# Kernel optimization log

Hardware: AMD Instinct MI355X
Metric: run time of the kernel (lower is better)

The kernel has to match this reference:

```python
import jax, jax.numpy as jnp
import numpy as np

T, A, H = 1024, 64, 2048

def setup_inputs() -> dict:
    key = jax.random.key(0)
    ks = jax.random.split(key, 12)
    s = 0.02
    return {
        "actions": jax.random.normal(ks[0], (T, A), jnp.float32),
        "state": jnp.zeros((1, H), jnp.float32),
        "W_ih": jax.random.normal(ks[1], (3 * H, A), jnp.float32) * s,
        "W_hh": jax.random.normal(ks[2], (3 * H, H), jnp.float32) * s,
        "b_ih": jax.random.normal(ks[3], (3 * H,), jnp.float32) * s,
        "b_hh": jax.random.normal(ks[4], (3 * H,), jnp.float32) * s,
        "fc1_w": jax.random.normal(ks[5], (H, H), jnp.float32) * s,
        "fc1_b": jax.random.normal(ks[6], (H,), jnp.float32) * s,
        "fc2_w": jax.random.normal(ks[7], (H, H), jnp.float32) * s,
        "fc2_b": jax.random.normal(ks[8], (H,), jnp.float32) * s,
        "mean_w": jax.random.normal(ks[9], (H, H), jnp.float32) * s,
        "mean_b": jnp.zeros((H,), jnp.float32),
        "std_w": jax.random.normal(ks[10], (H, H), jnp.float32) * s,
        "std_b": jnp.zeros((H,), jnp.float32),
    }

def reference(actions, state, W_ih, W_hh, b_ih, b_hh, fc1_w, fc1_b, fc2_w, fc2_b, mean_w, mean_b, std_w, std_b):
    def step(h, x):
        # torch GRUCell gate order: r, z, n
        gi = x[None] @ W_ih.T + b_ih          # [1, 3H]
        gh = h @ W_hh.T + b_hh                # [1, 3H]
        i_r, i_z, i_n = jnp.split(gi, 3, axis=-1)
        h_r, h_z, h_n = jnp.split(gh, 3, axis=-1)
        r = jax.nn.sigmoid(i_r + h_r)
        z = jax.nn.sigmoid(i_z + h_z)
        n = jnp.tanh(i_n + r * h_n)
        h_new = (1.0 - z) * n + z * h         # [1, H]
        s = jax.nn.elu(h_new)
        s = jax.nn.elu(s @ fc1_w.T + fc1_b)
        s = jax.nn.elu(s @ fc2_w.T + fc2_b)   # carried state for next step
        m = (s @ mean_w.T + mean_b)[0]        # [H]
        sd = jax.nn.softplus(s @ std_w.T + std_b)[0]
        return s, (m, sd)

    _, (means, stds) = jax.lax.scan(step, state, actions)
    return means, stds  # Normal(means, stds) parameters, each [T, H]
```

## Files before the change

kernel.cpp:

```cpp
#include <hip/hip_runtime.h>
#include <hip/hip_bf16.h>
#include <math.h>

#define T_STEPS 1024
#define HDIM    2048
#define ADIM    64
#define NBLK    256
#define NTHR    512
#define WPB     (NTHR / 64)

__device__ __forceinline__ float elu_f(float x)      { return x > 0.f ? x : expm1f(x); }
__device__ __forceinline__ float sigmoid_f(float x)  { return 1.f / (1.f + expf(-x)); }
__device__ __forceinline__ float softplus_f(float x) { return x > 0.f ? x + log1pf(expf(-x)) : log1pf(expf(x)); }

__device__ __forceinline__ unsigned long long cload64(const unsigned long long* p) {
    return __hip_atomic_load(p, __ATOMIC_RELAXED, __HIP_MEMORY_SCOPE_AGENT);
}
__device__ __forceinline__ void cstore64(unsigned long long* p, unsigned long long v) {
    __hip_atomic_store(p, v, __ATOMIC_RELAXED, __HIP_MEMORY_SCOPE_AGENT);
}
__device__ __forceinline__ unsigned long long pack_tag(unsigned tag, float v) {
    return ((unsigned long long)tag << 32) | (unsigned long long)__float_as_uint(v);
}

__device__ __forceinline__ void consume_vec(const unsigned long long* __restrict__ tg,
                                            unsigned tag, float* __restrict__ lsv) {
    const int i = threadIdx.x;
    unsigned pend = 0xFu;
    while (pend) {
        #pragma unroll
        for (int q = 0; q < 4; ++q) {
            if (pend & (1u << q)) {
                const unsigned long long x = cload64(tg + i + q * NTHR);
                if ((unsigned)(x >> 32) == tag) {
                    lsv[i + q * NTHR] = __uint_as_float((unsigned)x);
                    pend &= ~(1u << q);
                }
            }
        }
    }
    __syncthreads();
}

#define KEEP4(v) asm volatile("" : "+v"(v.x), "+v"(v.y), "+v"(v.z), "+v"(v.w))

__global__ void __launch_bounds__(NTHR, 2) gru_seq_kernel(
    const float* __restrict__ actions, const float* __restrict__ state,
    const float* __restrict__ W_ih, const float* __restrict__ W_hh,
    const float* __restrict__ b_ih, const float* __restrict__ b_hh,
    const float* __restrict__ fc1_w, const float* __restrict__ fc1_b,
    const float* __restrict__ fc2_w, const float* __restrict__ fc2_b,
    float* __restrict__ s_all,
    unsigned long long* __restrict__ tg0,
    unsigned long long* __restrict__ tg1,
    unsigned long long* __restrict__ tg2)
{
    __shared__ float lsv[HDIM];
    const int lane = threadIdx.x & 63;
    const int wave = threadIdx.x >> 6;
    const int j    = blockIdx.x * WPB + wave;

    float4 wr[8], wz[8], wn[8], f1[8], f2[8];
    {
        const float4* p0 = (const float4*)(W_hh + (size_t)j * HDIM);
        const float4* p1 = (const float4*)(W_hh + (size_t)(HDIM + j) * HDIM);
        const float4* p2 = (const float4*)(W_hh + (size_t)(2 * HDIM + j) * HDIM);
        const float4* p3 = (const float4*)(fc1_w + (size_t)j * HDIM);
        const float4* p4 = (const float4*)(fc2_w + (size_t)j * HDIM);
        #pragma unroll
        for (int i = 0; i < 8; ++i) {
            wr[i] = p0[i * 64 + lane]; KEEP4(wr[i]);
            wz[i] = p1[i * 64 + lane]; KEEP4(wz[i]);
            wn[i] = p2[i * 64 + lane]; KEEP4(wn[i]);
            f1[i] = p3[i * 64 + lane]; KEEP4(f1[i]);
            f2[i] = p4[i * 64 + lane]; KEEP4(f2[i]);
        }
    }
    const float wih_r = W_ih[(size_t)j * ADIM + lane];
    const float wih_z = W_ih[(size_t)(HDIM + j) * ADIM + lane];
    const float wih_n = W_ih[(size_t)(2 * HDIM + j) * ADIM + lane];
    const float bias_r = b_ih[j] + b_hh[j];
    const float bias_z = b_ih[HDIM + j] + b_hh[HDIM + j];
    const float bihn   = b_ih[2 * HDIM + j];
    const float bhhn   = b_hh[2 * HDIM + j];
    const float fb1    = fc1_b[j];
    const float fb2    = fc2_b[j];

    const float4* ls4 = (const float4*)lsv;

    for (int t = 0; t < T_STEPS; ++t) {
        const unsigned base = 3u * (unsigned)t;

        const float av = actions[t * ADIM + lane];
        if (t == 0) {
            #pragma unroll
            for (int q = 0; q < 4; ++q)
                lsv[threadIdx.x + q * NTHR] = state[threadIdx.x + q * NTHR];
            __syncthreads();
        } else {
            consume_vec(tg2, base, lsv);
        }
        {
            float dr = 0.f, dz = 0.f, dnH = 0.f;
            #pragma unroll
            for (int i = 0; i < 8; ++i) {
                const float4 s4 = ls4[i * 64 + lane];
                dr  += s4.x * wr[i].x + s4.y * wr[i].y + s4.z * wr[i].z + s4.w * wr[i].w;
                dz  += s4.x * wz[i].x + s4.y * wz[i].y + s4.z * wz[i].z + s4.w * wz[i].w;
                dnH += s4.x * wn[i].x + s4.y * wn[i].y + s4.z * wn[i].z + s4.w * wn[i].w;
            }
            float dnA = av * wih_n;
            dr += av * wih_r;
            dz += av * wih_z;
            #pragma unroll
            for (int m = 32; m > 0; m >>= 1) {
                dr  += __shfl_xor(dr, m, 64);
                dz  += __shfl_xor(dz, m, 64);
                dnH += __shfl_xor(dnH, m, 64);
                dnA += __shfl_xor(dnA, m, 64);
            }
            if (lane == 0) {
                const float r  = sigmoid_f(dr + bias_r);
                const float z  = sigmoid_f(dz + bias_z);
                const float n  = tanhf(dnA + bihn + r * (dnH + bhhn));
                const float hp = lsv[j];
                const float hn = (1.f - z) * n + z * hp;
                cstore64(&tg0[j], pack_tag(base + 1u, elu_f(hn)));
            }
        }
        __syncthreads();

        consume_vec(tg0, base + 1u, lsv);
        {
            float d1 = 0.f;
            #pragma unroll
            for (int i = 0; i < 8; ++i) {
                const float4 s4 = ls4[i * 64 + lane];
                d1 += s4.x * f1[i].x + s4.y * f1[i].y + s4.z * f1[i].z + s4.w * f1[i].w;
            }
            #pragma unroll
            for (int m = 32; m > 0; m >>= 1) d1 += __shfl_xor(d1, m, 64);
            if (lane == 0) cstore64(&tg1[j], pack_tag(base + 2u, elu_f(d1 + fb1)));
        }
        __syncthreads();

        consume_vec(tg1, base + 2u, lsv);
        {
            float d2 = 0.f;
            #pragma unroll
            for (int i = 0; i < 8; ++i) {
                const float4 s4 = ls4[i * 64 + lane];
                d2 += s4.x * f2[i].x + s4.y * f2[i].y + s4.z * f2[i].z + s4.w * f2[i].w;
            }
            #pragma unroll
            for (int m = 32; m > 0; m >>= 1) d2 += __shfl_xor(d2, m, 64);
            if (lane == 0) {
                const float v = elu_f(d2 + fb2);
                cstore64(&tg2[j], pack_tag(base + 3u, v));
                s_all[(size_t)t * HDIM + j] = v;
            }
        }
        __syncthreads();
    }
}

__global__ void __launch_bounds__(256) head_gemm_kernel(
    const float* __restrict__ s_all,
    const float* __restrict__ mean_w, const float* __restrict__ mean_b,
    const float* __restrict__ std_w,  const float* __restrict__ std_b,
    float* __restrict__ out)
{
    __shared__ float As[32 * 64];
    __shared__ float Bs[32 * 64];

    const int n0 = blockIdx.x * 64;
    const int t0 = blockIdx.y * 64;
    const bool is_std = (n0 >= HDIM);
    const float* W    = is_std ? std_w : mean_w;
    const float* bias = is_std ? std_b : mean_b;
    const int j0 = is_std ? (n0 - HDIM) : n0;

    const int tid = threadIdx.x;
    const int tx = tid & 15;
    const int ty = tid >> 4;

    float acc[4][4] = {};

    for (int k0 = 0; k0 < HDIM; k0 += 32) {
        __syncthreads();
        #pragma unroll
        for (int p = 0; p < 2; ++p) {
            const int id = tid + p * 256;
            const int m  = id >> 3;
            const int kk = id & 7;
            const float4 a = *(const float4*)&s_all[(size_t)(t0 + m) * HDIM + k0 + kk * 4];
            As[(kk * 4 + 0) * 64 + m] = a.x;
            As[(kk * 4 + 1) * 64 + m] = a.y;
            As[(kk * 4 + 2) * 64 + m] = a.z;
            As[(kk * 4 + 3) * 64 + m] = a.w;
            const float4 b = *(const float4*)&W[(size_t)(j0 + m) * HDIM + k0 + kk * 4];
            Bs[(kk * 4 + 0) * 64 + m] = b.x;
            Bs[(kk * 4 + 1) * 64 + m] = b.y;
            Bs[(kk * 4 + 2) * 64 + m] = b.z;
            Bs[(kk * 4 + 3) * 64 + m] = b.w;
        }
        __syncthreads();

        #pragma unroll
        for (int k = 0; k < 32; ++k) {
            const float4 a = *(const float4*)&As[k * 64 + ty * 4];
            const float4 b = *(const float4*)&Bs[k * 64 + tx * 4];
            const float am[4] = {a.x, a.y, a.z, a.w};
            const float bn[4] = {b.x, b.y, b.z, b.w};
            #pragma unroll
            for (int i = 0; i < 4; ++i)
                #pragma unroll
                for (int jj = 0; jj < 4; ++jj)
                    acc[i][jj] += am[i] * bn[jj];
        }
    }

    const size_t off = is_std ? (size_t)T_STEPS * HDIM : 0;
    #pragma unroll
    for (int i = 0; i < 4; ++i) {
        const int tt = t0 + ty * 4 + i;
        const int jc = j0 + tx * 4;
        float4 v;
        float* vp = (float*)&v;
        #pragma unroll
        for (int jj = 0; jj < 4; ++jj) {
            float val = acc[i][jj] + bias[jc + jj];
            if (is_std) val = softplus_f(val);
            vp[jj] = val;
        }
        *(float4*)&out[off + (size_t)tt * HDIM + jc] = v;
    }
}

extern "C" void kernel_launch(void* const* d_in, const int* in_sizes, int n_in,
                              void* d_out, int out_size, void* d_ws, size_t ws_size,
                              hipStream_t stream) {
    (void)in_sizes; (void)n_in; (void)out_size; (void)ws_size;
    const float* actions = (const float*)d_in[0];
    const float* state   = (const float*)d_in[1];
    const float* W_ih    = (const float*)d_in[2];
    const float* W_hh    = (const float*)d_in[3];
    const float* b_ih    = (const float*)d_in[4];
    const float* b_hh    = (const float*)d_in[5];
    const float* fc1_w   = (const float*)d_in[6];
    const float* fc1_b   = (const float*)d_in[7];
    const float* fc2_w   = (const float*)d_in[8];
    const float* fc2_b   = (const float*)d_in[9];
    const float* mean_w  = (const float*)d_in[10];
    const float* mean_b  = (const float*)d_in[11];
    const float* std_w   = (const float*)d_in[12];
    const float* std_b   = (const float*)d_in[13];
    float* out = (float*)d_out;

    float* s_all = (float*)d_ws;
    unsigned long long* tg0 = (unsigned long long*)(s_all + (size_t)T_STEPS * HDIM);
    unsigned long long* tg1 = tg0 + HDIM;
    unsigned long long* tg2 = tg1 + HDIM;

    void* args[] = { &actions, &state, &W_ih, &W_hh, &b_ih, &b_hh,
                     &fc1_w, &fc1_b, &fc2_w, &fc2_b,
                     &s_all, &tg0, &tg1, &tg2 };
    hipLaunchCooperativeKernel((const void*)gru_seq_kernel,
                               dim3(NBLK), dim3(NTHR), args, 0, stream);

    dim3 grid(4096 / 64, T_STEPS / 64);
    head_gemm_kernel<<<grid, 256, 0, stream>>>(s_all, mean_w, mean_b, std_w, std_b, out);
}
```

Measured before the change: 10.86 ms.

## Split each GRU row's dot product across two waves with 1024-thread blocks

Blocks now have 1024 threads. Each of the 8 rows per block is handled by two waves, each covering half of the K dimension, so every wave keeps half as many weight registers. The upper wave writes its partial sums to shared memory, and the lower wave adds them in and applies the nonlinearity. The aim is to shorten the per-wave dot-product latency and double the waves working on each step, at the cost of an extra barrier and a shared-memory exchange per phase. Launch bounds change to 4 waves per SIMD, which requires a tighter register budget.

Measured after the change: 17.39 ms. 1.6x slower.

```diff
diff --git a/kernel.cpp b/kernel.cpp
--- a/kernel.cpp
+++ b/kernel.cpp
@@ -6,8 +6,8 @@
 #define HDIM    2048
 #define ADIM    64
 #define NBLK    256
-#define NTHR    512
-#define WPB     (NTHR / 64)
+#define NTHR    1024
+#define ROWS_PB 8
 
 __device__ __forceinline__ float elu_f(float x)      { return x > 0.f ? x : expm1f(x); }
 __device__ __forceinline__ float sigmoid_f(float x)  { return 1.f / (1.f + expf(-x)); }
@@ -26,17 +26,15 @@
 __device__ __forceinline__ void consume_vec(const unsigned long long* __restrict__ tg,
                                             unsigned tag, float* __restrict__ lsv) {
     const int i = threadIdx.x;
-    unsigned pend = 0xFu;
+    unsigned pend = 3u;
     while (pend) {
-        #pragma unroll
-        for (int q = 0; q < 4; ++q) {
-            if (pend & (1u << q)) {
-                const unsigned long long x = cload64(tg + i + q * NTHR);
-                if ((unsigned)(x >> 32) == tag) {
-                    lsv[i + q * NTHR] = __uint_as_float((unsigned)x);
-                    pend &= ~(1u << q);
-                }
-            }
+        if (pend & 1u) {
+            const unsigned long long x = cload64(tg + i);
+            if ((unsigned)(x >> 32) == tag) { lsv[i] = __uint_as_float((unsigned)x); pend &= ~1u; }
+        }
+        if (pend & 2u) {
+            const unsigned long long x = cload64(tg + i + 1024);
+            if ((unsigned)(x >> 32) == tag) { lsv[i + 1024] = __uint_as_float((unsigned)x); pend &= ~2u; }
         }
     }
     __syncthreads();
@@ -44,7 +42,7 @@
 
 #define KEEP4(v) asm volatile("" : "+v"(v.x), "+v"(v.y), "+v"(v.z), "+v"(v.w))
 
-__global__ void __launch_bounds__(NTHR, 2) gru_seq_kernel(
+__global__ void __launch_bounds__(NTHR, 4) gru_seq_kernel(
     const float* __restrict__ actions, const float* __restrict__ state,
     const float* __restrict__ W_ih, const float* __restrict__ W_hh,
     const float* __restrict__ b_ih, const float* __restrict__ b_hh,
@@ -56,19 +54,25 @@
     unsigned long long* __restrict__ tg2)
 {
     __shared__ float lsv[HDIM];
-    const int lane = threadIdx.x & 63;
-    const int wave = threadIdx.x >> 6;
-    const int j    = blockIdx.x * WPB + wave;
-
-    float4 wr[8], wz[8], wn[8], f1[8], f2[8];
+    __shared__ float partU[ROWS_PB][3];
+
+    const int lane  = threadIdx.x & 63;
+    const int wave  = threadIdx.x >> 6;
+    const bool lower = (wave < ROWS_PB);
+    const int w8    = wave & (ROWS_PB - 1);
+    const int j     = blockIdx.x * ROWS_PB + w8;
+    const int c4    = lower ? 0 : 256;
+
+    float4 wr[4], wz[4], wn[4], f1[4], f2[4];
     {
-        const float4* p0 = (const float4*)(W_hh + (size_t)j * HDIM);
-        const float4* p1 = (const float4*)(W_hh + (size_t)(HDIM + j) * HDIM);
-        const float4* p2 = (const float4*)(W_hh + (size_t)(2 * HDIM + j) * HDIM);
-        const float4* p3 = (const float4*)(fc1_w + (size_t)j * HDIM);
-        const float4* p4 = (const float4*)(fc2_w + (size_t)j * HDIM);
-        #pragma unroll
-        for (int i = 0; i < 8; ++i) {
+        const int kbase = lower ? 0 : 1024;
+        const float4* p0 = (const float4*)(W_hh + (size_t)j * HDIM + kbase);
+        const float4* p1 = (const float4*)(W_hh + (size_t)(HDIM + j) * HDIM + kbase);
+        const float4* p2 = (const float4*)(W_hh + (size_t)(2 * HDIM + j) * HDIM + kbase);
+        const float4* p3 = (const float4*)(fc1_w + (size_t)j * HDIM + kbase);
+        const float4* p4 = (const float4*)(fc2_w + (size_t)j * HDIM + kbase);
+        #pragma unroll
+        for (int i = 0; i < 4; ++i) {
             wr[i] = p0[i * 64 + lane]; KEEP4(wr[i]);
             wz[i] = p1[i * 64 + lane]; KEEP4(wz[i]);
             wn[i] = p2[i * 64 + lane]; KEEP4(wn[i]);
@@ -76,42 +80,45 @@
             f2[i] = p4[i * 64 + lane]; KEEP4(f2[i]);
         }
     }
-    const float wih_r = W_ih[(size_t)j * ADIM + lane];
-    const float wih_z = W_ih[(size_t)(HDIM + j) * ADIM + lane];
-    const float wih_n = W_ih[(size_t)(2 * HDIM + j) * ADIM + lane];
-    const float bias_r = b_ih[j] + b_hh[j];
-    const float bias_z = b_ih[HDIM + j] + b_hh[HDIM + j];
-    const float bihn   = b_ih[2 * HDIM + j];
-    const float bhhn   = b_hh[2 * HDIM + j];
-    const float fb1    = fc1_b[j];
-    const float fb2    = fc2_b[j];
+    const float wih_r = lower ? W_ih[(size_t)j * ADIM + lane] : 0.f;
+    const float wih_z = lower ? W_ih[(size_t)(HDIM + j) * ADIM + lane] : 0.f;
+    const float wih_n = lower ? W_ih[(size_t)(2 * HDIM + j) * ADIM + lane] : 0.f;
+    const float bias_r = lower ? (b_ih[j] + b_hh[j]) : 0.f;
+    const float bias_z = lower ? (b_ih[HDIM + j] + b_hh[HDIM + j]) : 0.f;
+    const float bihn   = lower ? b_ih[2 * HDIM + j] : 0.f;
+    const float bhhn   = lower ? b_hh[2 * HDIM + j] : 0.f;
+    const float fb1    = lower ? fc1_b[j] : 0.f;
+    const float fb2    = lower ? fc2_b[j] : 0.f;
 
     const float4* ls4 = (const float4*)lsv;
 
     for (int t = 0; t < T_STEPS; ++t) {
         const unsigned base = 3u * (unsigned)t;
 
-        const float av = actions[t * ADIM + lane];
         if (t == 0) {
-            #pragma unroll
-            for (int q = 0; q < 4; ++q)
-                lsv[threadIdx.x + q * NTHR] = state[threadIdx.x + q * NTHR];
+            lsv[threadIdx.x]        = state[threadIdx.x];
+            lsv[threadIdx.x + 1024] = state[threadIdx.x + 1024];
             __syncthreads();
         } else {
             consume_vec(tg2, base, lsv);
         }
+        const float hp = lsv[j];
         {
             float dr = 0.f, dz = 0.f, dnH = 0.f;
             #pragma unroll
-            for (int i = 0; i < 8; ++i) {
-                const float4 s4 = ls4[i * 64 + lane];
+            for (int i = 0; i < 4; ++i) {
+                const float4 s4 = ls4[c4 + i * 64 + lane];
                 dr  += s4.x * wr[i].x + s4.y * wr[i].y + s4.z * wr[i].z + s4.w * wr[i].w;
                 dz  += s4.x * wz[i].x + s4.y * wz[i].y + s4.z * wz[i].z + s4.w * wz[i].w;
                 dnH += s4.x * wn[i].x + s4.y * wn[i].y + s4.z * wn[i].z + s4.w * wn[i].w;
             }
-            float dnA = av * wih_n;
-            dr += av * wih_r;
-            dz += av * wih_z;
+            float dnA = 0.f;
+            if (lower) {
+                const float av = actions[t * ADIM + lane];
+                dr += av * wih_r;
+                dz += av * wih_z;
+                dnA = av * wih_n;
+            }
             #pragma unroll
             for (int m = 32; m > 0; m >>= 1) {
                 dr  += __shfl_xor(dr, m, 64);
@@ -119,48 +126,56 @@
                 dnH += __shfl_xor(dnH, m, 64);
                 dnA += __shfl_xor(dnA, m, 64);
             }
-            if (lane == 0) {
-                const float r  = sigmoid_f(dr + bias_r);
-                const float z  = sigmoid_f(dz + bias_z);
-                const float n  = tanhf(dnA + bihn + r * (dnH + bhhn));
-                const float hp = lsv[j];
+            if (!lower && lane == 0) {
+                partU[w8][0] = dr; partU[w8][1] = dz; partU[w8][2] = dnH;
+            }
+            __syncthreads();
+            if (lower && lane == 0) {
+                const float drT  = dr  + partU[w8][0];
+                const float dzT  = dz  + partU[w8][1];
+                const float dnHT = dnH + partU[w8][2];
+                const float r  = sigmoid_f(drT + bias_r);
+                const float z  = sigmoid_f(dzT + bias_z);
+                const float n  = tanhf(dnA + bihn + r * (dnHT + bhhn));
                 const float hn = (1.f - z) * n + z * hp;
                 cstore64(&tg0[j], pack_tag(base + 1u, elu_f(hn)));
             }
         }
-        __syncthreads();
 
         consume_vec(tg0, base + 1u, lsv);
         {
             float d1 = 0.f;
             #pragma unroll
-            for (int i = 0; i < 8; ++i) {
-                const float4 s4 = ls4[i * 64 + lane];
+            for (int i = 0; i < 4; ++i) {
+                const float4 s4 = ls4[c4 + i * 64 + lane];
                 d1 += s4.x * f1[i].x + s4.y * f1[i].y + s4.z * f1[i].z + s4.w * f1[i].w;
             }
             #pragma unroll
             for (int m = 32; m > 0; m >>= 1) d1 += __shfl_xor(d1, m, 64);
-            if (lane == 0) cstore64(&tg1[j], pack_tag(base + 2u, elu_f(d1 + fb1)));
-        }
-        __syncthreads();
+            if (!lower && lane == 0) partU[w8][0] = d1;
+            __syncthreads();
+            if (lower && lane == 0)
+                cstore64(&tg1[j], pack_tag(base + 2u, elu_f(d1 + partU[w8][0] + fb1)));
+        }
 
         consume_vec(tg1, base + 2u, lsv);
         {
             float d2 = 0.f;
             #pragma unroll
-            for (int i = 0; i < 8; ++i) {
-                const float4 s4 = ls4[i * 64 + lane];
+            for (int i = 0; i < 4; ++i) {
+                const float4 s4 = ls4[c4 + i * 64 + lane];
                 d2 += s4.x * f2[i].x + s4.y * f2[i].y + s4.z * f2[i].z + s4.w * f2[i].w;
             }
             #pragma unroll
             for (int m = 32; m > 0; m >>= 1) d2 += __shfl_xor(d2, m, 64);
-            if (lane == 0) {
-                const float v = elu_f(d2 + fb2);
+            if (!lower && lane == 0) partU[w8][0] = d2;
+            __syncthreads();
+            if (lower && lane == 0) {
+                const float v = elu_f(d2 + partU[w8][0] + fb2);
                 cstore64(&tg2[j], pack_tag(base + 3u, v));
                 s_all[(size_t)t * HDIM + j] = v;
             }
         }
-        __syncthreads();
     }
 }
 
```

## Store recurrent weights as bf16 in LDS and poll flags with cache-bypassing vector loads

Applied to the files above, without the earlier changes.

Moves the persistent W_hh, fc1 and most of fc2 weights out of registers into 156KB of LDS as packed bf16, with a tail of fc2 kept in fp32 registers. Launch bounds drop to one block per CU. Flag polling now uses inline-asm global_load_dwordx4 with sc0 sc1, reading two tag/value pairs per load, and the trailing __syncthreads are folded into consume_vec. The aim is to free registers and cut per-step synchronisation latency in the serial recurrence. In exchange, bf16 weights lose precision over 1024 recurrent steps and every step now reads weights from LDS.

After: 13.81 ms. +27.1%, slower.

```diff
diff --git a/kernel.cpp b/kernel.cpp
--- a/kernel.cpp
+++ b/kernel.cpp
@@ -7,44 +7,73 @@
 #define ADIM    64
 #define NBLK    256
 #define NTHR    512
-#define WPB     (NTHR / 64)
+#define WPB     8
+
+typedef unsigned int u32;
+typedef unsigned int uint4v __attribute__((ext_vector_type(4)));
+
+#define SMEM_BYTES 159744
+#define FC2_U32    32768
+#define LSV_BYTES  151552
 
 __device__ __forceinline__ float elu_f(float x)      { return x > 0.f ? x : expm1f(x); }
 __device__ __forceinline__ float sigmoid_f(float x)  { return 1.f / (1.f + expf(-x)); }
 __device__ __forceinline__ float softplus_f(float x) { return x > 0.f ? x + log1pf(expf(-x)) : log1pf(expf(x)); }
 
-__device__ __forceinline__ unsigned long long cload64(const unsigned long long* p) {
-    return __hip_atomic_load(p, __ATOMIC_RELAXED, __HIP_MEMORY_SCOPE_AGENT);
-}
-__device__ __forceinline__ void cstore64(unsigned long long* p, unsigned long long v) {
-    __hip_atomic_store(p, v, __ATOMIC_RELAXED, __HIP_MEMORY_SCOPE_AGENT);
-}
-__device__ __forceinline__ unsigned long long pack_tag(unsigned tag, float v) {
-    return ((unsigned long long)tag << 32) | (unsigned long long)__float_as_uint(v);
+__device__ __forceinline__ u32 bf16rne(float x) {
+    u32 u = __float_as_uint(x);
+    return (u + 0x7fffu + ((u >> 16) & 1u)) >> 16;
+}
+__device__ __forceinline__ u32 pack_bf16(float lo, float hi) {
+    return bf16rne(lo) | (bf16rne(hi) << 16);
+}
+__device__ __forceinline__ float blo(u32 u) { return __uint_as_float(u << 16); }
+__device__ __forceinline__ float bhi(u32 u) { return __uint_as_float(u & 0xffff0000u); }
+
+__device__ __forceinline__ void cstore64(unsigned long long* p, u32 tag, float v) {
+    unsigned long long x = ((unsigned long long)tag << 32) | (unsigned long long)__float_as_uint(v);
+    __hip_atomic_store(p, x, __ATOMIC_RELAXED, __HIP_MEMORY_SCOPE_AGENT);
+}
+
+__device__ __forceinline__ void bypass_load2(uint4v& a, uint4v& b,
+                                             const unsigned long long* pa,
+                                             const unsigned long long* pb) {
+    asm volatile("global_load_dwordx4 %0, %2, off sc0 sc1\n\t"
+                 "global_load_dwordx4 %1, %3, off sc0 sc1\n\t"
+                 "s_waitcnt vmcnt(0)"
+                 : "=v"(a), "=v"(b)
+                 : "v"(pa), "v"(pb));
 }
 
 __device__ __forceinline__ void consume_vec(const unsigned long long* __restrict__ tg,
-                                            unsigned tag, float* __restrict__ lsv) {
+                                            u32 tag, float* __restrict__ lsv) {
+    __syncthreads();
     const int i = threadIdx.x;
-    unsigned pend = 0xFu;
-    while (pend) {
-        #pragma unroll
-        for (int q = 0; q < 4; ++q) {
-            if (pend & (1u << q)) {
-                const unsigned long long x = cload64(tg + i + q * NTHR);
-                if ((unsigned)(x >> 32) == tag) {
-                    lsv[i + q * NTHR] = __uint_as_float((unsigned)x);
-                    pend &= ~(1u << q);
-                }
-            }
-        }
+    const unsigned long long* pa = tg + 2 * i;
+    const unsigned long long* pb = tg + 1024 + 2 * i;
+    uint4v a, b;
+    bypass_load2(a, b, pa, pb);
+    u32 pend = 0xFu;
+    for (;;) {
+        if ((pend & 1u) && a.y == tag) { lsv[2*i]        = __uint_as_float(a.x); pend &= ~1u; }
+        if ((pend & 2u) && a.w == tag) { lsv[2*i+1]      = __uint_as_float(a.z); pend &= ~2u; }
+        if ((pend & 4u) && b.y == tag) { lsv[1024+2*i]   = __uint_as_float(b.x); pend &= ~4u; }
+        if ((pend & 8u) && b.w == tag) { lsv[1025+2*i]   = __uint_as_float(b.z); pend &= ~8u; }
+        if (!pend) break;
+        if (pend & 3u)
+            asm volatile("global_load_dwordx4 %0, %1, off sc0 sc1" : "=v"(a) : "v"(pa));
+        if (pend & 12u)
+            asm volatile("global_load_dwordx4 %0, %1, off sc0 sc1" : "=v"(b) : "v"(pb));
+        asm volatile("s_waitcnt vmcnt(0)");
     }
     __syncthreads();
 }
 
-#define KEEP4(v) asm volatile("" : "+v"(v.x), "+v"(v.y), "+v"(v.z), "+v"(v.w))
-
-__global__ void __launch_bounds__(NTHR, 2) gru_seq_kernel(
+#define DOT8(acc, wv, s0, s1)                                                  \
+    acc += blo(wv.x)*s0.x + bhi(wv.x)*s0.y + blo(wv.y)*s0.z + bhi(wv.y)*s0.w   \
+         + blo(wv.z)*s1.x + bhi(wv.z)*s1.y + blo(wv.w)*s1.z + bhi(wv.w)*s1.w
+
+__global__ void __launch_bounds__(NTHR, 1) gru_seq_kernel(
     const float* __restrict__ actions, const float* __restrict__ state,
     const float* __restrict__ W_ih, const float* __restrict__ W_hh,
     const float* __restrict__ b_ih, const float* __restrict__ b_hh,
@@ -55,27 +84,35 @@
     unsigned long long* __restrict__ tg1,
     unsigned long long* __restrict__ tg2)
 {
-    __shared__ float lsv[HDIM];
-    const int lane = threadIdx.x & 63;
-    const int wave = threadIdx.x >> 6;
+    extern __shared__ __align__(16) unsigned char smem[];
+    u32*   lwu = (u32*)smem;
+    float* lsv = (float*)(smem + LSV_BYTES);
+    const float4* ls4 = (const float4*)lsv;
+
+    const int tid  = threadIdx.x;
+    const int lane = tid & 63;
+    const int wave = tid >> 6;
     const int j    = blockIdx.x * WPB + wave;
 
-    float4 wr[8], wz[8], wn[8], f1[8], f2[8];
-    {
-        const float4* p0 = (const float4*)(W_hh + (size_t)j * HDIM);
-        const float4* p1 = (const float4*)(W_hh + (size_t)(HDIM + j) * HDIM);
-        const float4* p2 = (const float4*)(W_hh + (size_t)(2 * HDIM + j) * HDIM);
-        const float4* p3 = (const float4*)(fc1_w + (size_t)j * HDIM);
-        const float4* p4 = (const float4*)(fc2_w + (size_t)j * HDIM);
-        #pragma unroll
-        for (int i = 0; i < 8; ++i) {
-            wr[i] = p0[i * 64 + lane]; KEEP4(wr[i]);
-            wz[i] = p1[i * 64 + lane]; KEEP4(wz[i]);
-            wn[i] = p2[i * 64 + lane]; KEEP4(wn[i]);
-            f1[i] = p3[i * 64 + lane]; KEEP4(f1[i]);
-            f2[i] = p4[i * 64 + lane]; KEEP4(f2[i]);
-        }
-    }
+    for (int g = 0; g < 4; ++g) {
+        const float* basep = (g < 3) ? (W_hh + ((size_t)g * HDIM + (size_t)blockIdx.x * WPB) * HDIM)
+                                     : (fc1_w + (size_t)blockIdx.x * WPB * HDIM);
+        for (int p = tid; p < 8192; p += NTHR) {
+            const int r = p >> 10, cu = p & 1023;
+            const float2 v = *(const float2*)&basep[(size_t)r * HDIM + 2 * cu];
+            lwu[g * 8192 + p] = pack_bf16(v.x, v.y);
+        }
+    }
+    for (int p = tid; p < 5120; p += NTHR) {
+        const int r = p / 640, cu = p % 640;
+        const float2 v = *(const float2*)&fc2_w[((size_t)blockIdx.x * WPB + r) * HDIM + 2 * cu];
+        lwu[FC2_U32 + p] = pack_bf16(v.x, v.y);
+    }
+    float f2t[12];
+    #pragma unroll
+    for (int c = 0; c < 12; ++c)
+        f2t[c] = fc2_w[(size_t)j * HDIM + 1280 + c * 64 + lane];
+
     const float wih_r = W_ih[(size_t)j * ADIM + lane];
     const float wih_z = W_ih[(size_t)(HDIM + j) * ADIM + lane];
     const float wih_n = W_ih[(size_t)(2 * HDIM + j) * ADIM + lane];
@@ -85,17 +122,22 @@
     const float bhhn   = b_hh[2 * HDIM + j];
     const float fb1    = fc1_b[j];
     const float fb2    = fc2_b[j];
-
-    const float4* ls4 = (const float4*)lsv;
+    __syncthreads();
+
+    const u32* rowR = lwu + 0 * 8192 + wave * 1024;
+    const u32* rowZ = lwu + 1 * 8192 + wave * 1024;
+    const u32* rowN = lwu + 2 * 8192 + wave * 1024;
+    const u32* row1 = lwu + 3 * 8192 + wave * 1024;
+    const u32* row2 = lwu + FC2_U32 + wave * 640;
 
     for (int t = 0; t < T_STEPS; ++t) {
-        const unsigned base = 3u * (unsigned)t;
-
+        const u32 base = 3u * (u32)t;
         const float av = actions[t * ADIM + lane];
+
         if (t == 0) {
             #pragma unroll
             for (int q = 0; q < 4; ++q)
-                lsv[threadIdx.x + q * NTHR] = state[threadIdx.x + q * NTHR];
+                lsv[tid + q * NTHR] = state[tid + q * NTHR];
             __syncthreads();
         } else {
             consume_vec(tg2, base, lsv);
@@ -103,11 +145,16 @@
         {
             float dr = 0.f, dz = 0.f, dnH = 0.f;
             #pragma unroll
-            for (int i = 0; i < 8; ++i) {
-                const float4 s4 = ls4[i * 64 + lane];
-                dr  += s4.x * wr[i].x + s4.y * wr[i].y + s4.z * wr[i].z + s4.w * wr[i].w;
-                dz  += s4.x * wz[i].x + s4.y * wz[i].y + s4.z * wz[i].z + s4.w * wz[i].w;
-                dnH += s4.x * wn[i].x + s4.y * wn[i].y + s4.z * wn[i].z + s4.w * wn[i].w;
+            for (int i = 0; i < 4; ++i) {
+                const int ui = i * 256 + lane * 4;
+                const uint4v wa = *(const uint4v*)&rowR[ui];
+                const uint4v wb = *(const uint4v*)&rowZ[ui];
+                const uint4v wc = *(const uint4v*)&rowN[ui];
+                const float4 s0 = ls4[i * 128 + lane * 2];
+                const float4 s1 = ls4[i * 128 + lane * 2 + 1];
+                DOT8(dr, wa, s0, s1);
+                DOT8(dz, wb, s0, s1);
+                DOT8(dnH, wc, s0, s1);
             }
             float dnA = av * wih_n;
             dr += av * wih_r;
@@ -125,42 +172,53 @@
                 const float n  = tanhf(dnA + bihn + r * (dnH + bhhn));
                 const float hp = lsv[j];
                 const float hn = (1.f - z) * n + z * hp;
-                cstore64(&tg0[j], pack_tag(base + 1u, elu_f(hn)));
-            }
-        }
-        __syncthreads();
+                cstore64(&tg0[j], base + 1u, elu_f(hn));
+            }
+        }
 
         consume_vec(tg0, base + 1u, lsv);
         {
             float d1 = 0.f;
             #pragma unroll
-            for (int i = 0; i < 8; ++i) {
-                const float4 s4 = ls4[i * 64 + lane];
-                d1 += s4.x * f1[i].x + s4.y * f1[i].y + s4.z * f1[i].z + s4.w * f1[i].w;
+            for (int i = 0; i < 4; ++i) {
+                const int ui = i * 256 + lane * 4;
+                const uint4v wv = *(const uint4v*)&row1[ui];
+                const float4 s0 = ls4[i * 128 + lane * 2];
+                const float4 s1 = ls4[i * 128 + lane * 2 + 1];
+                DOT8(d1, wv, s0, s1);
             }
             #pragma unroll
             for (int m = 32; m > 0; m >>= 1) d1 += __shfl_xor(d1, m, 64);
-            if (lane == 0) cstore64(&tg1[j], pack_tag(base + 2u, elu_f(d1 + fb1)));
-        }
-        __syncthreads();
+            if (lane == 0) cstore64(&tg1[j], base + 2u, elu_f(d1 + fb1));
+        }
 
         consume_vec(tg1, base + 2u, lsv);
         {
             float d2 = 0.f;
             #pragma unroll
-            for (int i = 0; i < 8; ++i) {
-                const float4 s4 = ls4[i * 64 + lane];
-                d2 += s4.x * f2[i].x + s4.y * f2[i].y + s4.z * f2[i].z + s4.w * f2[i].w;
-            }
+            for (int i = 0; i < 2; ++i) {
+                const int ui = i * 256 + lane * 4;
+                const uint4v wv = *(const uint4v*)&row2[ui];
+                const float4 s0 = ls4[i * 128 + lane * 2];
+                const float4 s1 = ls4[i * 128 + lane * 2 + 1];
+                DOT8(d2, wv, s0, s1);
+            }
+            {
+                const uint2 wv = *(const uint2*)&row2[512 + lane * 2];
+                const float4 s0 = ls4[256 + lane];
+                d2 += blo(wv.x)*s0.x + bhi(wv.x)*s0.y + blo(wv.y)*s0.z + bhi(wv.y)*s0.w;
+            }
+            #pragma unroll
+            for (int c = 0; c < 12; ++c)
+                d2 += f2t[c] * lsv[1280 + c * 64 + lane];
             #pragma unroll
             for (int m = 32; m > 0; m >>= 1) d2 += __shfl_xor(d2, m, 64);
             if (lane == 0) {
                 const float v = elu_f(d2 + fb2);
-                cstore64(&tg2[j], pack_tag(base + 3u, v));
+                cstore64(&tg2[j], base + 3u, v);
                 s_all[(size_t)t * HDIM + j] = v;
             }
         }
-        __syncthreads();
     }
 }
 
@@ -262,11 +320,14 @@
     unsigned long long* tg1 = tg0 + HDIM;
     unsigned long long* tg2 = tg1 + HDIM;
 
+    (void)hipFuncSetAttribute((const void*)gru_seq_kernel,
+                              hipFuncAttributeMaxDynamicSharedMemorySize, SMEM_BYTES);
+
     void* args[] = { &actions, &state, &W_ih, &W_hh, &b_ih, &b_hh,
                      &fc1_w, &fc1_b, &fc2_w, &fc2_b,
                      &s_all, &tg0, &tg1, &tg2 };
     hipLaunchCooperativeKernel((const void*)gru_seq_kernel,
-                               dim3(NBLK), dim3(NTHR), args, 0, stream);
+                               dim3(NBLK), dim3(NTHR), args, SMEM_BYTES, stream);
 
     dim3 grid(4096 / 64, T_STEPS / 64);
     head_gemm_kernel<<<grid, 256, 0, stream>>>(s_all, mean_w, mean_b, std_w, std_b, out);
```
